# Performance work log

Hardware: AMD Instinct MI355X
Metric: run time of the kernel (lower is better)

## Reference

```python
import jax, jax.numpy as jnp
import numpy as np

BN_EPS = 1e-5


def setup_inputs() -> dict:
    key = jax.random.key(0)
    ks = jax.random.split(key, 13)
    B, C, H, W = 8, 256, 96, 32
    D = C // 2  # inter_channels
    s = 0.05
    return {
        "x": jax.random.normal(ks[0], (B, C, H, W), jnp.float32),
        "g_w": jax.random.normal(ks[1], (D, C), jnp.float32) * s,
        "g_b": jax.random.normal(ks[2], (D,), jnp.float32) * s,
        "theta_w": jax.random.normal(ks[3], (D, C), jnp.float32) * s,
        "theta_b": jax.random.normal(ks[4], (D,), jnp.float32) * s,
        "phi_w": jax.random.normal(ks[5], (D, C), jnp.float32) * s,
        "phi_b": jax.random.normal(ks[6], (D,), jnp.float32) * s,
        "w_w": jax.random.normal(ks[7], (C, D), jnp.float32) * s,
        "w_b": jax.random.normal(ks[8], (C,), jnp.float32) * s,
        "bn_gamma": jax.random.normal(ks[9], (C,), jnp.float32),
        "bn_beta": jax.random.normal(ks[10], (C,), jnp.float32) * s,
        "bn_mean": jax.random.normal(ks[11], (C,), jnp.float32) * s,
        "bn_var": jax.random.uniform(ks[12], (C,), jnp.float32),
    }


def reference(x, g_w, g_b, theta_w, theta_b, phi_w, phi_b, w_w, w_b,
              bn_gamma, bn_beta, bn_mean, bn_var):
    B, C, H, W = x.shape
    N = H * W
    xf = x.reshape(B, C, N)  # flatten spatial: (B, C, N)

    # 1x1 conv projections == per-pixel linear maps
    g_x = jnp.einsum('dc,bcn->bnd', g_w, xf) + g_b            # (B, N, D)
    theta_x = jnp.einsum('dc,bcn->bnd', theta_w, xf) + theta_b  # (B, N, D)
    phi_x = jnp.einsum('dc,bcn->bdn', phi_w, xf) + phi_b[:, None]  # (B, D, N)

    # unnormalized attention: f = theta phi^T / N, then y = f g
    f_div_C = jnp.einsum('bnd,bdm->bnm', theta_x, phi_x) / N  # (B, N, N)
    y = jnp.einsum('bnm,bmd->bnd', f_div_C, g_x)              # (B, N, D)

    # output 1x1 conv + eval-mode BatchNorm2d
    wy = jnp.einsum('cd,bnd->bcn', w_w, y) + w_b[:, None]     # (B, C, N)
    inv = bn_gamma / jnp.sqrt(bn_var + BN_EPS)
    wy = (wy - bn_mean[:, None]) * inv[:, None] + bn_beta[:, None]

    z = wy.reshape(B, C, H, W) + x  # residual
    return z
```

## Files before the change

### kernel.cpp

```cpp
#include <hip/hip_runtime.h>
#include <hip/hip_bf16.h>
#include <cstddef>

typedef __attribute__((ext_vector_type(8))) short short8;
typedef __attribute__((ext_vector_type(4))) float floatx4;
typedef __hip_bfloat16 bf16;

#define NB 8
#define NC 256
#define ND 128
#define NN 3072
#define NBLK 48
#define BN_EPS 1e-5f

static __device__ __forceinline__ short f2s(float v) {
    bf16 h = __float2bfloat16(v);
    return *reinterpret_cast<short*>(&h);
}

__global__ __launch_bounds__(256) void setup_kernel(
    const float* __restrict__ phi_w, const float* __restrict__ g_w,
    const float* __restrict__ theta_w, short* __restrict__ Wall)
{
    int t = threadIdx.x;
    int r = blockIdx.x;
    const float* src = (r < 128) ? (phi_w + (size_t)r * NC)
                     : (r < 256) ? (g_w + (size_t)(r - 128) * NC)
                                 : (theta_w + (size_t)(r - 256) * NC);
    Wall[(size_t)r * NC + t] = f2s(src[t]);
}

__global__ __launch_bounds__(384)
void proj_kernel(const float* __restrict__ x, const short* __restrict__ Wall,
                 const float* __restrict__ phi_b, const float* __restrict__ g_b,
                 const float* __restrict__ theta_b,
                 short* __restrict__ thDN, float* __restrict__ Mpart)
{
    __shared__ short PGs[256][72];
    __shared__ short Xs[64][72];
    int b = blockIdx.y;
    int n0 = blockIdx.x * 64;
    int t = threadIdx.x;
    int lane = t & 63;
    int wave = t >> 6;
    int lm = lane & 15;
    int lk = (lane >> 4) * 8;

    const float* xb = x + (size_t)b * NC * NN;

    floatx4 zero = {0.f, 0.f, 0.f, 0.f};
    floatx4 acc[4][4];
#pragma unroll
    for (int i = 0; i < 4; ++i)
#pragma unroll
        for (int j = 0; j < 4; ++j) acc[i][j] = zero;

#pragma unroll
    for (int kt = 0; kt < NC; kt += 64) {
        __syncthreads();
        if (t < 256) {
            int sn = t & 63, cg = t >> 6;
            const float* src = xb + (size_t)(kt + cg * 16) * NN + n0 + sn;
            short8 s0, s1;
#pragma unroll
            for (int j = 0; j < 8; ++j) {
                s0[j] = f2s(src[(size_t)j * NN]);
                s1[j] = f2s(src[(size_t)(8 + j) * NN]);
            }
            *(short8*)&Xs[sn][cg * 16]     = s0;
            *(short8*)&Xs[sn][cg * 16 + 8] = s1;
        }
        __syncthreads();
#pragma unroll
        for (int kk = 0; kk < 64; kk += 32) {
            short8 af[4], bfr[4];
#pragma unroll
            for (int i = 0; i < 4; ++i)
                af[i] = *(const short8*)(Wall +
                        (size_t)(wave * 64 + i * 16 + lm) * NC + kt + kk + lk);
#pragma unroll
            for (int j = 0; j < 4; ++j)
                bfr[j] = *(const short8*)&Xs[j * 16 + lm][kk + lk];
#pragma unroll
            for (int i = 0; i < 4; ++i)
#pragma unroll
                for (int j = 0; j < 4; ++j)
                    acc[i][j] = __builtin_amdgcn_mfma_f32_16x16x32_bf16(
                        af[i], bfr[j], acc[i][j], 0, 0, 0);
        }
    }

    int row0 = wave * 64 + (lane >> 4) * 4;

    if (wave < 4) {
#pragma unroll
        for (int i = 0; i < 4; ++i) {
#pragma unroll
            for (int r = 0; r < 4; ++r) {
                int row = row0 + i * 16 + r;
                float bv = (row < 128) ? phi_b[row] : g_b[row - 128];
#pragma unroll
                for (int j = 0; j < 4; ++j)
                    PGs[row][lm + j * 16] = f2s(acc[i][j][r] + bv);
            }
        }
    } else {
        short* Tb = thDN + (size_t)b * ND * NN;
#pragma unroll
        for (int i = 0; i < 4; ++i) {
#pragma unroll
            for (int r = 0; r < 4; ++r) {
                int d = row0 - 256 + i * 16 + r;
                float bv = theta_b[d];
#pragma unroll
                for (int j = 0; j < 4; ++j)
                    Tb[(size_t)d * NN + n0 + lm + j * 16] =
                        f2s(acc[i][j][r] + bv);
            }
        }
    }
    __syncthreads();

    if (wave < 4) {
        int wr = wave >> 1, wc = wave & 1;
        floatx4 macc[4][4];
#pragma unroll
        for (int i = 0; i < 4; ++i)
#pragma unroll
            for (int j = 0; j < 4; ++j) macc[i][j] = zero;
#pragma unroll
        for (int kk = 0; kk < 64; kk += 32) {
            short8 af[4], bfr[4];
#pragma unroll
            for (int i = 0; i < 4; ++i)
                af[i] = *(const short8*)&PGs[wr * 64 + i * 16 + lm][kk + lk];
#pragma unroll
            for (int j = 0; j < 4; ++j)
                bfr[j] = *(const short8*)&PGs[128 + wc * 64 + j * 16 + lm][kk + lk];
#pragma unroll
            for (int i = 0; i < 4; ++i)
#pragma unroll
                for (int j = 0; j < 4; ++j)
                    macc[i][j] = __builtin_amdgcn_mfma_f32_16x16x32_bf16(
                        af[i], bfr[j], macc[i][j], 0, 0, 0);
        }
        float* Mf = Mpart + ((size_t)b * NBLK + blockIdx.x) * (ND * ND);
        int mr0 = wr * 64 + (lane >> 4) * 4;
        int mc0 = wc * 64 + lm;
        const float sc = 1.f / (float)NN;
#pragma unroll
        for (int i = 0; i < 4; ++i)
#pragma unroll
            for (int j = 0; j < 4; ++j)
#pragma unroll
                for (int r = 0; r < 4; ++r)
                    Mf[(size_t)(mr0 + i * 16 + r) * ND + mc0 + j * 16] =
                        macc[i][j][r] * sc;
    }
}

__global__ __launch_bounds__(256)
void reduce_kernel(const float* __restrict__ Mpart, short* __restrict__ Mb16)
{
    int idx = blockIdx.x * 256 + threadIdx.x;
    int b = idx >> 14;
    int e = idx & 16383;
    const float* src = Mpart + (size_t)b * NBLK * 16384 + e;
    float s = 0.f;
#pragma unroll 8
    for (int p = 0; p < NBLK; ++p) s += src[(size_t)p * 16384];
    Mb16[(size_t)b * 16384 + e] = f2s(s);
}

__global__ __launch_bounds__(256)
void final_kernel(const short* __restrict__ Mb16, const short* __restrict__ thDN,
                  const float* __restrict__ w_w, const float* __restrict__ w_b,
                  const float* __restrict__ gamma, const float* __restrict__ beta,
                  const float* __restrict__ mean, const float* __restrict__ var,
                  const float* __restrict__ x, float* __restrict__ out)
{
    __shared__ short As[128][72];
    __shared__ short Bs[128][72];
    __shared__ short P2s[128][136];
    int b = blockIdx.z;
    int tile_m = blockIdx.y * 128;
    int tile_n = blockIdx.x * 128;
    int t = threadIdx.x;
    int lane = t & 63;
    int wave = t >> 6;
    int wr = wave >> 1, wc = wave & 1;
    int lm = lane & 15;
    int lk = (lane >> 4) * 8;
    int ch = (t & 7) * 8;
    int r0 = t >> 3;

    const short* Mb = Mb16 + (size_t)b * ND * ND;

    floatx4 zero = {0.f, 0.f, 0.f, 0.f};
    floatx4 acc[4][4];
#pragma unroll
    for (int i = 0; i < 4; ++i)
#pragma unroll
        for (int j = 0; j < 4; ++j) acc[i][j] = zero;

#pragma unroll
    for (int kt = 0; kt < ND; kt += 64) {
        __syncthreads();
#pragma unroll
        for (int p = 0; p < 4; ++p) {
            int r = r0 + p * 32;
            const float* ap = w_w + (size_t)(tile_m + r) * ND + kt + ch;
            floatx4 a0 = *(const floatx4*)ap, a1 = *(const floatx4*)(ap + 4);
            short8 sa;
#pragma unroll
            for (int j = 0; j < 4; ++j) { sa[j] = f2s(a0[j]); sa[4 + j] = f2s(a1[j]); }
            *(short8*)&As[r][ch] = sa;
            *(short8*)&Bs[r][ch] = *(const short8*)(Mb + (size_t)r * ND + kt + ch);
        }
        __syncthreads();
#pragma unroll
        for (int kk = 0; kk < 64; kk += 32) {
            short8 af[4], bfr[4];
#pragma unroll
            for (int i = 0; i < 4; ++i)
                af[i] = *(const short8*)&As[wr * 64 + i * 16 + lm][kk + lk];
#pragma unroll
            for (int j = 0; j < 4; ++j)
                bfr[j] = *(const short8*)&Bs[wc * 64 + j * 16 + lm][kk + lk];
#pragma unroll
            for (int i = 0; i < 4; ++i)
#pragma unroll
                for (int j = 0; j < 4; ++j)
                    acc[i][j] = __builtin_amdgcn_mfma_f32_16x16x32_bf16(
                        af[i], bfr[j], acc[i][j], 0, 0, 0);
        }
    }

    {
        int row0 = wr * 64 + (lane >> 4) * 4;
        int col0 = wc * 64 + lm;
#pragma unroll
        for (int i = 0; i < 4; ++i) {
#pragma unroll
            for (int r = 0; r < 4; ++r) {
                int cl = row0 + i * 16 + r;
                int c = tile_m + cl;
                float iv = gamma[c] * rsqrtf(var[c] + BN_EPS);
#pragma unroll
                for (int j = 0; j < 4; ++j)
                    P2s[cl][col0 + j * 16] = f2s(acc[i][j][r] * iv);
            }
        }
    }

    floatx4 acc2[4][4];
#pragma unroll
    for (int i = 0; i < 4; ++i)
#pragma unroll
        for (int j = 0; j < 4; ++j) acc2[i][j] = zero;

    const short* Tb = thDN + (size_t)b * ND * NN;
#pragma unroll
    for (int kt = 0; kt < ND; kt += 64) {
        __syncthreads();
        {
            int dl = t & 63;
            int ng = t >> 6;
            const short* src = Tb + (size_t)(kt + dl) * NN + tile_n + ng * 32;
#pragma unroll
            for (int q = 0; q < 4; ++q) {
                short8 v = *(const short8*)(src + q * 8);
#pragma unroll
                for (int jj = 0; jj < 8; ++jj)
                    Bs[ng * 32 + q * 8 + jj][dl] = v[jj];
            }
        }
        __syncthreads();
#pragma unroll
        for (int kk = 0; kk < 64; kk += 32) {
            short8 af[4], bfr[4];
#pragma unroll
            for (int i = 0; i < 4; ++i)
                af[i] = *(const short8*)&P2s[wr * 64 + i * 16 + lm][kt + kk + lk];
#pragma unroll
            for (int j = 0; j < 4; ++j)
                bfr[j] = *(const short8*)&Bs[wc * 64 + j * 16 + lm][kk + lk];
#pragma unroll
            for (int i = 0; i < 4; ++i)
#pragma unroll
                for (int j = 0; j < 4; ++j)
                    acc2[i][j] = __builtin_amdgcn_mfma_f32_16x16x32_bf16(
                        af[i], bfr[j], acc2[i][j], 0, 0, 0);
        }
    }

    int crow0 = tile_m + wr * 64 + (lane >> 4) * 4;
    int col0 = tile_n + wc * 64 + lm;
    float* Cf = out + (size_t)b * NC * NN;
    const float* Rg = x + (size_t)b * NC * NN;
#pragma unroll
    for (int i = 0; i < 4; ++i) {
#pragma unroll
        for (int r = 0; r < 4; ++r) {
            int c = crow0 + i * 16 + r;
            float iv = gamma[c] * rsqrtf(var[c] + BN_EPS);
            float b2 = iv * (w_b[c] - mean[c]) + beta[c];
#pragma unroll
            for (int j = 0; j < 4; ++j) {
                size_t idx = (size_t)c * NN + col0 + j * 16;
                Cf[idx] = acc2[i][j][r] + b2 + Rg[idx];
            }
        }
    }
}

extern "C" void kernel_launch(void* const* d_in, const int* in_sizes, int n_in,
                              void* d_out, int out_size, void* d_ws, size_t ws_size,
                              hipStream_t stream)
{
    const float* x       = (const float*)d_in[0];
    const float* g_w     = (const float*)d_in[1];
    const float* g_b     = (const float*)d_in[2];
    const float* theta_w = (const float*)d_in[3];
    const float* theta_b = (const float*)d_in[4];
    const float* phi_w   = (const float*)d_in[5];
    const float* phi_b   = (const float*)d_in[6];
    const float* w_w     = (const float*)d_in[7];
    const float* w_b     = (const float*)d_in[8];
    const float* gamma   = (const float*)d_in[9];
    const float* beta    = (const float*)d_in[10];
    const float* mean    = (const float*)d_in[11];
    const float* var     = (const float*)d_in[12];
    (void)in_sizes; (void)n_in; (void)out_size; (void)ws_size;

    char* w = (char*)d_ws;
    short* thDN  = (short*)w; w += (size_t)NB * ND * NN * 2;
    float* Mpart = (float*)w; w += (size_t)NB * NBLK * ND * ND * 4;
    short* Mb16  = (short*)w; w += (size_t)NB * ND * ND * 2;
    short* Wall  = (short*)w; w += (size_t)384 * NC * 2;

    setup_kernel<<<dim3(384), dim3(256), 0, stream>>>(
        phi_w, g_w, theta_w, Wall);

    proj_kernel<<<dim3(NN / 64, NB), dim3(384), 0, stream>>>(
        x, Wall, phi_b, g_b, theta_b, thDN, Mpart);

    reduce_kernel<<<dim3(512), dim3(256), 0, stream>>>(Mpart, Mb16);

    final_kernel<<<dim3(NN / 128, NC / 128, NB), 256, 0, stream>>>(
        Mb16, thDN, w_w, w_b, gamma, beta, mean, var, x, (float*)d_out);
}
```

Measured before the change: 137.8 us.

## Fuse all stages into one cooperative mega-kernel with grid syncs

Replaces the four-kernel pipeline (weight conversion, projection, partial-M reduction, final GEMMs) with a single cooperative kernel of 256 blocks that synchronises the grid between phases. Weights are converted to bf16 inside the kernel, theta is stored transposed (N x D) so the final GEMM reads it directly from global memory without an LDS transpose, and the x loads for the next K step are issued before the current step's MFMAs. The partial-M reduction and the w_w·M product are spread across blocks, and each block writes a slice of P2 to global memory. This removes launch overhead and intermediate kernels, at the cost of grid-wide barriers, reliance on cooperative-launch co-residency, and only 256 blocks of 512 threads to fill the device.

```diff
diff --git a/kernel.cpp b/kernel.cpp
--- a/kernel.cpp
+++ b/kernel.cpp
@@ -1,8 +1,12 @@
 #include <hip/hip_runtime.h>
 #include <hip/hip_bf16.h>
+#include <hip/hip_cooperative_groups.h>
 #include <cstddef>
 
+namespace cg = cooperative_groups;
+
 typedef __attribute__((ext_vector_type(8))) short short8;
+typedef __attribute__((ext_vector_type(4))) short short4v;
 typedef __attribute__((ext_vector_type(4))) float floatx4;
 typedef __hip_bfloat16 bf16;
 
@@ -10,7 +14,8 @@
 #define NC 256
 #define ND 128
 #define NN 3072
-#define NBLK 48
+#define NT1 96
+#define TILES 32
 #define BN_EPS 1e-5f
 
 static __device__ __forceinline__ short f2s(float v) {
@@ -18,297 +23,274 @@
     return *reinterpret_cast<short*>(&h);
 }
 
-__global__ __launch_bounds__(256) void setup_kernel(
-    const float* __restrict__ phi_w, const float* __restrict__ g_w,
-    const float* __restrict__ theta_w, short* __restrict__ Wall)
+union SMem {
+    struct { short Ws[384][72]; short Xs[96][72]; } p1;
+    struct { short PGs[256][104]; } p1e;
+    struct { short As[256][136]; short Ms[16][136]; } p2;
+};
+
+__global__ __launch_bounds__(512, 2)
+void mega_kernel(const float* __restrict__ x,
+                 const float* __restrict__ g_w, const float* __restrict__ g_b,
+                 const float* __restrict__ theta_w, const float* __restrict__ theta_b,
+                 const float* __restrict__ phi_w, const float* __restrict__ phi_b,
+                 const float* __restrict__ w_w, const float* __restrict__ w_b,
+                 const float* __restrict__ gamma, const float* __restrict__ beta,
+                 const float* __restrict__ mean, const float* __restrict__ var,
+                 short* __restrict__ thT, float* __restrict__ Mpart,
+                 short* __restrict__ P2g, float* __restrict__ out)
 {
-    int t = threadIdx.x;
-    int r = blockIdx.x;
-    const float* src = (r < 128) ? (phi_w + (size_t)r * NC)
-                     : (r < 256) ? (g_w + (size_t)(r - 128) * NC)
-                                 : (theta_w + (size_t)(r - 256) * NC);
-    Wall[(size_t)r * NC + t] = f2s(src[t]);
-}
-
-__global__ __launch_bounds__(384)
-void proj_kernel(const float* __restrict__ x, const short* __restrict__ Wall,
-                 const float* __restrict__ phi_b, const float* __restrict__ g_b,
-                 const float* __restrict__ theta_b,
-                 short* __restrict__ thDN, float* __restrict__ Mpart)
-{
-    __shared__ short PGs[256][72];
-    __shared__ short Xs[64][72];
-    int b = blockIdx.y;
-    int n0 = blockIdx.x * 64;
+    __shared__ SMem sm;
+    cg::grid_group grid = cg::this_grid();
+
     int t = threadIdx.x;
     int lane = t & 63;
     int wave = t >> 6;
     int lm = lane & 15;
-    int lk = (lane >> 4) * 8;
-
-    const float* xb = x + (size_t)b * NC * NN;
+    int lh = lane >> 4;
+    int lk = lh * 8;
+
+    int b = blockIdx.x >> 5;
+    int tile = blockIdx.x & 31;
+    int n0 = tile * NT1;
 
     floatx4 zero = {0.f, 0.f, 0.f, 0.f};
-    floatx4 acc[4][4];
-#pragma unroll
-    for (int i = 0; i < 4; ++i)
-#pragma unroll
-        for (int j = 0; j < 4; ++j) acc[i][j] = zero;
-
-#pragma unroll
-    for (int kt = 0; kt < NC; kt += 64) {
+
+    {
+        const float* xb = x + (size_t)b * NC * NN;
+
+        floatx4 acc[3][6];
+#pragma unroll
+        for (int i = 0; i < 3; ++i)
+#pragma unroll
+            for (int j = 0; j < 6; ++j) acc[i][j] = zero;
+
+        int sn = t % 96;
+        int cgp = t / 96;
+        float xf[16];
+        if (t < 384) {
+#pragma unroll
+            for (int j = 0; j < 16; ++j)
+                xf[j] = xb[(size_t)(cgp * 16 + j) * NN + n0 + sn];
+        }
+
+#pragma unroll
+        for (int kt = 0; kt < NC; kt += 64) {
+            __syncthreads();
+#pragma unroll
+            for (int i = 0; i < 12; ++i) {
+                int idx = t + i * 512;
+                int row = idx >> 4;
+                int c4 = (idx & 15) * 4;
+                const float* sp = (row < 128) ? phi_w + (size_t)row * NC
+                                : (row < 256) ? g_w + (size_t)(row - 128) * NC
+                                              : theta_w + (size_t)(row - 256) * NC;
+                floatx4 v = *(const floatx4*)(sp + kt + c4);
+                short4v o;
+#pragma unroll
+                for (int j = 0; j < 4; ++j) o[j] = f2s(v[j]);
+                *(short4v*)&sm.p1.Ws[row][c4] = o;
+            }
+            if (t < 384) {
+                short8 s0, s1;
+#pragma unroll
+                for (int j = 0; j < 8; ++j) {
+                    s0[j] = f2s(xf[j]);
+                    s1[j] = f2s(xf[8 + j]);
+                }
+                *(short8*)&sm.p1.Xs[sn][cgp * 16]     = s0;
+                *(short8*)&sm.p1.Xs[sn][cgp * 16 + 8] = s1;
+            }
+            __syncthreads();
+            if (t < 384 && kt < NC - 64) {
+#pragma unroll
+                for (int j = 0; j < 16; ++j)
+                    xf[j] = xb[(size_t)(kt + 64 + cgp * 16 + j) * NN + n0 + sn];
+            }
+#pragma unroll
+            for (int h = 0; h < 64; h += 32) {
+                short8 af[3], bfr[6];
+#pragma unroll
+                for (int i = 0; i < 3; ++i)
+                    af[i] = *(const short8*)&sm.p1.Ws[wave * 48 + i * 16 + lm][h + lk];
+#pragma unroll
+                for (int j = 0; j < 6; ++j)
+                    bfr[j] = *(const short8*)&sm.p1.Xs[j * 16 + lm][h + lk];
+#pragma unroll
+                for (int i = 0; i < 3; ++i)
+#pragma unroll
+                    for (int j = 0; j < 6; ++j)
+                        acc[i][j] = __builtin_amdgcn_mfma_f32_16x16x32_bf16(
+                            af[i], bfr[j], acc[i][j], 0, 0, 0);
+            }
+        }
+
         __syncthreads();
-        if (t < 256) {
-            int sn = t & 63, cg = t >> 6;
-            const float* src = xb + (size_t)(kt + cg * 16) * NN + n0 + sn;
-            short8 s0, s1;
-#pragma unroll
-            for (int j = 0; j < 8; ++j) {
-                s0[j] = f2s(src[(size_t)j * NN]);
-                s1[j] = f2s(src[(size_t)(8 + j) * NN]);
-            }
-            *(short8*)&Xs[sn][cg * 16]     = s0;
-            *(short8*)&Xs[sn][cg * 16 + 8] = s1;
+        int row_base = wave * 48 + lh * 4;
+#pragma unroll
+        for (int i = 0; i < 3; ++i) {
+#pragma unroll
+            for (int r = 0; r < 4; ++r) {
+                int row = row_base + i * 16 + r;
+                if (row < 256) {
+                    float bv = (row < 128) ? phi_b[row] : g_b[row - 128];
+#pragma unroll
+                    for (int j = 0; j < 6; ++j)
+                        sm.p1e.PGs[row][j * 16 + lm] = f2s(acc[i][j][r] + bv);
+                } else {
+                    int d = row - 256;
+                    float bv = theta_b[d];
+                    short* Tp = thT + ((size_t)b * NN + n0 + lm) * ND + d;
+#pragma unroll
+                    for (int j = 0; j < 6; ++j)
+                        Tp[(size_t)(j * 16) * ND] = f2s(acc[i][j][r] + bv);
+                }
+            }
         }
         __syncthreads();
-#pragma unroll
-        for (int kk = 0; kk < 64; kk += 32) {
-            short8 af[4], bfr[4];
+
+        {
+            int wr = wave >> 2;
+            int wc = wave & 3;
+            floatx4 macc[4][2];
 #pragma unroll
             for (int i = 0; i < 4; ++i)
-                af[i] = *(const short8*)(Wall +
-                        (size_t)(wave * 64 + i * 16 + lm) * NC + kt + kk + lk);
-#pragma unroll
-            for (int j = 0; j < 4; ++j)
-                bfr[j] = *(const short8*)&Xs[j * 16 + lm][kk + lk];
+#pragma unroll
+                for (int j = 0; j < 2; ++j) macc[i][j] = zero;
+#pragma unroll
+            for (int kk = 0; kk < 96; kk += 32) {
+                short8 af[4], bfr[2];
+#pragma unroll
+                for (int i = 0; i < 4; ++i)
+                    af[i] = *(const short8*)&sm.p1e.PGs[wr * 64 + i * 16 + lm][kk + lk];
+#pragma unroll
+                for (int j = 0; j < 2; ++j)
+                    bfr[j] = *(const short8*)&sm.p1e.PGs[128 + wc * 32 + j * 16 + lm][kk + lk];
+#pragma unroll
+                for (int i = 0; i < 4; ++i)
+#pragma unroll
+                    for (int j = 0; j < 2; ++j)
+                        macc[i][j] = __builtin_amdgcn_mfma_f32_16x16x32_bf16(
+                            af[i], bfr[j], macc[i][j], 0, 0, 0);
+            }
+            float* Mf = Mpart + (size_t)blockIdx.x * (ND * ND);
+            const float sc = 1.f / (float)NN;
 #pragma unroll
             for (int i = 0; i < 4; ++i)
 #pragma unroll
-                for (int j = 0; j < 4; ++j)
-                    acc[i][j] = __builtin_amdgcn_mfma_f32_16x16x32_bf16(
-                        af[i], bfr[j], acc[i][j], 0, 0, 0);
+                for (int j = 0; j < 2; ++j)
+#pragma unroll
+                    for (int r = 0; r < 4; ++r)
+                        Mf[(size_t)(wr * 64 + i * 16 + lh * 4 + r) * ND
+                           + wc * 32 + j * 16 + lm] = macc[i][j][r] * sc;
         }
     }
 
-    int row0 = wave * 64 + (lane >> 4) * 4;
-
-    if (wave < 4) {
-#pragma unroll
-        for (int i = 0; i < 4; ++i) {
-#pragma unroll
-            for (int r = 0; r < 4; ++r) {
-                int row = row0 + i * 16 + r;
-                float bv = (row < 128) ? phi_b[row] : g_b[row - 128];
-#pragma unroll
-                for (int j = 0; j < 4; ++j)
-                    PGs[row][lm + j * 16] = f2s(acc[i][j][r] + bv);
-            }
-        }
-    } else {
-        short* Tb = thDN + (size_t)b * ND * NN;
-#pragma unroll
-        for (int i = 0; i < 4; ++i) {
-#pragma unroll
-            for (int r = 0; r < 4; ++r) {
-                int d = row0 - 256 + i * 16 + r;
-                float bv = theta_b[d];
-#pragma unroll
-                for (int j = 0; j < 4; ++j)
-                    Tb[(size_t)d * NN + n0 + lm + j * 16] =
-                        f2s(acc[i][j][r] + bv);
+    grid.sync();
+    {
+        int e0 = tile * 4;
+#pragma unroll
+        for (int i = 0; i < 16; ++i) {
+            int idx = t + i * 512;
+            int c = idx >> 5;
+            int d4 = (idx & 31) * 4;
+            floatx4 v = *(const floatx4*)(w_w + (size_t)idx * 4);
+            short4v o;
+#pragma unroll
+            for (int j = 0; j < 4; ++j) o[j] = f2s(v[j]);
+            *(short4v*)&sm.p2.As[c][d4] = o;
+        }
+        if (t < 384) {
+            short4v z = {0, 0, 0, 0};
+            *(short4v*)&sm.p2.Ms[4 + (t >> 5)][(t & 31) * 4] = z;
+        }
+        if (t < 128) {
+            int e = t >> 5;
+            int d4 = (t & 31) * 4;
+            const float* src = Mpart + (size_t)b * (TILES * ND * ND)
+                             + (size_t)(e0 + e) * ND + d4;
+            floatx4 s = zero;
+#pragma unroll 8
+            for (int p = 0; p < TILES; ++p)
+                s += *(const floatx4*)(src + (size_t)p * (ND * ND));
+            short4v o;
+#pragma unroll
+            for (int j = 0; j < 4; ++j) o[j] = f2s(s[j]);
+            *(short4v*)&sm.p2.Ms[e][d4] = o;
+        }
+        __syncthreads();
+        floatx4 pacc[2];
+        pacc[0] = zero; pacc[1] = zero;
+#pragma unroll
+        for (int kk = 0; kk < 128; kk += 32) {
+            short8 bfr = *(const short8*)&sm.p2.Ms[lm][kk + lk];
+#pragma unroll
+            for (int i = 0; i < 2; ++i) {
+                short8 af = *(const short8*)&sm.p2.As[wave * 32 + i * 16 + lm][kk + lk];
+                pacc[i] = __builtin_amdgcn_mfma_f32_16x16x32_bf16(
+                    af, bfr, pacc[i], 0, 0, 0);
+            }
+        }
+        if (lm < 4) {
+            int e = e0 + lm;
+#pragma unroll
+            for (int i = 0; i < 2; ++i) {
+#pragma unroll
+                for (int r = 0; r < 4; ++r) {
+                    int c = wave * 32 + i * 16 + lh * 4 + r;
+                    float iv = gamma[c] * rsqrtf(var[c] + BN_EPS);
+                    P2g[((size_t)b * NC + c) * ND + e] = f2s(pacc[i][r] * iv);
+                }
             }
         }
     }
-    __syncthreads();
-
-    if (wave < 4) {
-        int wr = wave >> 1, wc = wave & 1;
-        floatx4 macc[4][4];
+
+    grid.sync();
+    {
+        int wr = wave >> 1;
+        int wc = wave & 1;
+        const short* P2b = P2g + (size_t)b * NC * ND;
+        const short* Tb = thT + (size_t)b * NN * ND;
+
+        floatx4 acc2[4][3];
 #pragma unroll
         for (int i = 0; i < 4; ++i)
 #pragma unroll
-            for (int j = 0; j < 4; ++j) macc[i][j] = zero;
-#pragma unroll
-        for (int kk = 0; kk < 64; kk += 32) {
-            short8 af[4], bfr[4];
+            for (int j = 0; j < 3; ++j) acc2[i][j] = zero;
+
+#pragma unroll
+        for (int kk = 0; kk < 128; kk += 32) {
+            short8 af[4], bfr[3];
 #pragma unroll
             for (int i = 0; i < 4; ++i)
-                af[i] = *(const short8*)&PGs[wr * 64 + i * 16 + lm][kk + lk];
-#pragma unroll
-            for (int j = 0; j < 4; ++j)
-                bfr[j] = *(const short8*)&PGs[128 + wc * 64 + j * 16 + lm][kk + lk];
+                af[i] = *(const short8*)(P2b
+                        + (size_t)(wr * 64 + i * 16 + lm) * ND + kk + lk);
+#pragma unroll
+            for (int j = 0; j < 3; ++j)
+                bfr[j] = *(const short8*)(Tb
+                        + (size_t)(n0 + wc * 48 + j * 16 + lm) * ND + kk + lk);
 #pragma unroll
             for (int i = 0; i < 4; ++i)
 #pragma unroll
-                for (int j = 0; j < 4; ++j)
-                    macc[i][j] = __builtin_amdgcn_mfma_f32_16x16x32_bf16(
-                        af[i], bfr[j], macc[i][j], 0, 0, 0);
-        }
-        float* Mf = Mpart + ((size_t)b * NBLK + blockIdx.x) * (ND * ND);
-        int mr0 = wr * 64 + (lane >> 4) * 4;
-        int mc0 = wc * 64 + lm;
-        const float sc = 1.f / (float)NN;
-#pragma unroll
-        for (int i = 0; i < 4; ++i)
-#pragma unroll
-            for (int j = 0; j < 4; ++j)
-#pragma unroll
-                for (int r = 0; r < 4; ++r)
-                    Mf[(size_t)(mr0 + i * 16 + r) * ND + mc0 + j * 16] =
-                        macc[i][j][r] * sc;
-    }
-}
-
-__global__ __launch_bounds__(256)
-void reduce_kernel(const float* __restrict__ Mpart, short* __restrict__ Mb16)
-{
-    int idx = blockIdx.x * 256 + threadIdx.x;
-    int b = idx >> 14;
-    int e = idx & 16383;
-    const float* src = Mpart + (size_t)b * NBLK * 16384 + e;
-    float s = 0.f;
-#pragma unroll 8
-    for (int p = 0; p < NBLK; ++p) s += src[(size_t)p * 16384];
-    Mb16[(size_t)b * 16384 + e] = f2s(s);
-}
-
-__global__ __launch_bounds__(256)
-void final_kernel(const short* __restrict__ Mb16, const short* __restrict__ thDN,
-                  const float* __restrict__ w_w, const float* __restrict__ w_b,
-                  const float* __restrict__ gamma, const float* __restrict__ beta,
-                  const float* __restrict__ mean, const float* __restrict__ var,
-                  const float* __restrict__ x, float* __restrict__ out)
-{
-    __shared__ short As[128][72];
-    __shared__ short Bs[128][72];
-    __shared__ short P2s[128][136];
-    int b = blockIdx.z;
-    int tile_m = blockIdx.y * 128;
-    int tile_n = blockIdx.x * 128;
-    int t = threadIdx.x;
-    int lane = t & 63;
-    int wave = t >> 6;
-    int wr = wave >> 1, wc = wave & 1;
-    int lm = lane & 15;
-    int lk = (lane >> 4) * 8;
-    int ch = (t & 7) * 8;
-    int r0 = t >> 3;
-
-    const short* Mb = Mb16 + (size_t)b * ND * ND;
-
-    floatx4 zero = {0.f, 0.f, 0.f, 0.f};
-    floatx4 acc[4][4];
-#pragma unroll
-    for (int i = 0; i < 4; ++i)
-#pragma unroll
-        for (int j = 0; j < 4; ++j) acc[i][j] = zero;
-
-#pragma unroll
-    for (int kt = 0; kt < ND; kt += 64) {
-        __syncthreads();
-#pragma unroll
-        for (int p = 0; p < 4; ++p) {
-            int r = r0 + p * 32;
-            const float* ap = w_w + (size_t)(tile_m + r) * ND + kt + ch;
-            floatx4 a0 = *(const floatx4*)ap, a1 = *(const floatx4*)(ap + 4);
-            short8 sa;
-#pragma unroll
-            for (int j = 0; j < 4; ++j) { sa[j] = f2s(a0[j]); sa[4 + j] = f2s(a1[j]); }
-            *(short8*)&As[r][ch] = sa;
-            *(short8*)&Bs[r][ch] = *(const short8*)(Mb + (size_t)r * ND + kt + ch);
-        }
-        __syncthreads();
-#pragma unroll
-        for (int kk = 0; kk < 64; kk += 32) {
-            short8 af[4], bfr[4];
-#pragma unroll
-            for (int i = 0; i < 4; ++i)
-                af[i] = *(const short8*)&As[wr * 64 + i * 16 + lm][kk + lk];
-#pragma unroll
-            for (int j = 0; j < 4; ++j)
-                bfr[j] = *(const short8*)&Bs[wc * 64 + j * 16 + lm][kk + lk];
-#pragma unroll
-            for (int i = 0; i < 4; ++i)
-#pragma unroll
-                for (int j = 0; j < 4; ++j)
-                    acc[i][j] = __builtin_amdgcn_mfma_f32_16x16x32_bf16(
-                        af[i], bfr[j], acc[i][j], 0, 0, 0);
-        }
-    }
-
-    {
-        int row0 = wr * 64 + (lane >> 4) * 4;
-        int col0 = wc * 64 + lm;
-#pragma unroll
-        for (int i = 0; i < 4; ++i) {
-#pragma unroll
-            for (int r = 0; r < 4; ++r) {
-                int cl = row0 + i * 16 + r;
-                int c = tile_m + cl;
-                float iv = gamma[c] * rsqrtf(var[c] + BN_EPS);
-#pragma unroll
-                for (int j = 0; j < 4; ++j)
-                    P2s[cl][col0 + j * 16] = f2s(acc[i][j][r] * iv);
-            }
-        }
-    }
-
-    floatx4 acc2[4][4];
-#pragma unroll
-    for (int i = 0; i < 4; ++i)
-#pragma unroll
-        for (int j = 0; j < 4; ++j) acc2[i][j] = zero;
-
-    const short* Tb = thDN + (size_t)b * ND * NN;
-#pragma unroll
-    for (int kt = 0; kt < ND; kt += 64) {
-        __syncthreads();
-        {
-            int dl = t & 63;
-            int ng = t >> 6;
-            const short* src = Tb + (size_t)(kt + dl) * NN + tile_n + ng * 32;
-#pragma unroll
-            for (int q = 0; q < 4; ++q) {
-                short8 v = *(const short8*)(src + q * 8);
-#pragma unroll
-                for (int jj = 0; jj < 8; ++jj)
-                    Bs[ng * 32 + q * 8 + jj][dl] = v[jj];
-            }
-        }
-        __syncthreads();
-#pragma unroll
-        for (int kk = 0; kk < 64; kk += 32) {
-            short8 af[4], bfr[4];
-#pragma unroll
-            for (int i = 0; i < 4; ++i)
-                af[i] = *(const short8*)&P2s[wr * 64 + i * 16 + lm][kt + kk + lk];
-#pragma unroll
-            for (int j = 0; j < 4; ++j)
-                bfr[j] = *(const short8*)&Bs[wc * 64 + j * 16 + lm][kk + lk];
-#pragma unroll
-            for (int i = 0; i < 4; ++i)
-#pragma unroll
-                for (int j = 0; j < 4; ++j)
+                for (int j = 0; j < 3; ++j)
                     acc2[i][j] = __builtin_amdgcn_mfma_f32_16x16x32_bf16(
                         af[i], bfr[j], acc2[i][j], 0, 0, 0);
         }
-    }
-
-    int crow0 = tile_m + wr * 64 + (lane >> 4) * 4;
-    int col0 = tile_n + wc * 64 + lm;
-    float* Cf = out + (size_t)b * NC * NN;
-    const float* Rg = x + (size_t)b * NC * NN;
-#pragma unroll
-    for (int i = 0; i < 4; ++i) {
-#pragma unroll
-        for (int r = 0; r < 4; ++r) {
-            int c = crow0 + i * 16 + r;
-            float iv = gamma[c] * rsqrtf(var[c] + BN_EPS);
-            float b2 = iv * (w_b[c] - mean[c]) + beta[c];
-#pragma unroll
-            for (int j = 0; j < 4; ++j) {
-                size_t idx = (size_t)c * NN + col0 + j * 16;
-                Cf[idx] = acc2[i][j][r] + b2 + Rg[idx];
+
+        float* Cf = out + (size_t)b * NC * NN;
+        const float* Rg = x + (size_t)b * NC * NN;
+#pragma unroll
+        for (int i = 0; i < 4; ++i) {
+#pragma unroll
+            for (int r = 0; r < 4; ++r) {
+                int c = wr * 64 + i * 16 + lh * 4 + r;
+                float iv = gamma[c] * rsqrtf(var[c] + BN_EPS);
+                float b2 = iv * (w_b[c] - mean[c]) + beta[c];
+#pragma unroll
+                for (int j = 0; j < 3; ++j) {
+                    size_t idx = (size_t)c * NN + n0 + wc * 48 + j * 16 + lm;
+                    Cf[idx] = acc2[i][j][r] + b2 + Rg[idx];
+                }
             }
         }
     }
@@ -334,19 +316,17 @@
     (void)in_sizes; (void)n_in; (void)out_size; (void)ws_size;
 
     char* w = (char*)d_ws;
-    short* thDN  = (short*)w; w += (size_t)NB * ND * NN * 2;
-    float* Mpart = (float*)w; w += (size_t)NB * NBLK * ND * ND * 4;
-    short* Mb16  = (short*)w; w += (size_t)NB * ND * ND * 2;
-    short* Wall  = (short*)w; w += (size_t)384 * NC * 2;
-
-    setup_kernel<<<dim3(384), dim3(256), 0, stream>>>(
-        phi_w, g_w, theta_w, Wall);
-
-    proj_kernel<<<dim3(NN / 64, NB), dim3(384), 0, stream>>>(
-        x, Wall, phi_b, g_b, theta_b, thDN, Mpart);
-
-    reduce_kernel<<<dim3(512), dim3(256), 0, stream>>>(Mpart, Mb16);
-
-    final_kernel<<<dim3(NN / 128, NC / 128, NB), 256, 0, stream>>>(
-        Mb16, thDN, w_w, w_b, gamma, beta, mean, var, x, (float*)d_out);
+    short* thT   = (short*)w; w += (size_t)NB * NN * ND * 2;
+    float* Mpart = (float*)w; w += (size_t)NB * TILES * ND * ND * 4;
+    short* P2g   = (short*)w; w += (size_t)NB * NC * ND * 2;
+    float* outp  = (float*)d_out;
+
+    void* kargs[] = {
+        (void*)&x, (void*)&g_w, (void*)&g_b, (void*)&theta_w, (void*)&theta_b,
+        (void*)&phi_w, (void*)&phi_b, (void*)&w_w, (void*)&w_b,
+        (void*)&gamma, (void*)&beta, (void*)&mean, (void*)&var,
+        (void*)&thT, (void*)&Mpart, (void*)&P2g, (void*)&outp
+    };
+    hipLaunchCooperativeKernel((void*)mega_kernel, dim3(NB * TILES), dim3(512),
+                               kargs, 0, stream);
 }
```

Measured after the change: 222.1 us. 61.1% more time.
